# Kernel tuning notes

Measured on AMD Instinct MI355X. Metric: run time of the kernel, lower is better.

The kernel has to match this reference:

```python
import jax, jax.numpy as jnp
import numpy as np

NHEAD = 16


def setup_inputs() -> dict:
    key = jax.random.key(0)
    ks = jax.random.split(key, 6)
    S, B, D = 2048, 2, 1024
    std = float(np.sqrt(6.0 / (D + D)))  # xavier_uniform bound
    inp = {
        "query": jax.random.normal(ks[0], (S, B, D), jnp.float32),
        "key": jax.random.normal(ks[1], (S, B, D), jnp.float32),
        "value": jax.random.normal(ks[2], (S, B, D), jnp.float32),
        "Wq": jax.random.uniform(ks[3], (D, D), jnp.float32, -std, std),
        "bq": jnp.ones((D,), jnp.float32),
        "Wk": jax.random.uniform(ks[4], (D, D), jnp.float32, -std, std),
        "bk": jnp.ones((D,), jnp.float32),
        "Wv": jax.random.uniform(ks[5], (D, D), jnp.float32, -std, std),
        "bv": jnp.ones((D,), jnp.float32),
    }
    return inp


def reference(query, key, value, Wq, bq, Wk, bk, Wv, bv):
    S, B, D = query.shape
    h = NHEAD
    d = D // h
    scale = jnp.asarray(d ** 0.5, query.dtype)
    # projections (nn.Linear: x @ W^T + b)
    q = (query @ Wq.T + bq).reshape(S, B, h, d)
    k = (key @ Wk.T + bk).reshape(S, B, h, d)
    v = (value @ Wv.T + bv).reshape(S, B, h, d)
    # batch_first=False path: scores [b,h,i,j], softmax over j, then AV
    scores = jnp.einsum('ibhd,jbhd->bhij', q, k) / scale
    attn = jax.nn.softmax(scores, axis=-1)
    out = jnp.einsum('bhij,jbhd->ibhd', attn, v).reshape(S, B, D)
    return out
```

## Files before the change

kernel.cpp:

```cpp
#include <hip/hip_runtime.h>
#include <hip/hip_bf16.h>

#define S_LEN 2048
#define BATCH 2
#define DMODEL 1024
#define NHEAD 16
#define HDIM 64
#define MTOT (S_LEN * BATCH)
#define QKV_ELEMS ((size_t)MTOT * DMODEL)
#define XOFF (3 * QKV_ELEMS)
#define WOFF (XOFF + 3 * QKV_ELEMS)
#define WSEG ((size_t)DMODEL * DMODEL)

typedef __bf16 bf16x8 __attribute__((ext_vector_type(8)));
typedef unsigned short u16x8 __attribute__((ext_vector_type(8)));
typedef float f32x4 __attribute__((ext_vector_type(4)));
typedef float f32x16 __attribute__((ext_vector_type(16)));
typedef unsigned int u32x4 __attribute__((ext_vector_type(4)));

__device__ __forceinline__ unsigned short f2bf(float f) {
    unsigned int u = __float_as_uint(f);
    u += 0x7FFFu + ((u >> 16) & 1u);
    return (unsigned short)(u >> 16);
}

__device__ __forceinline__ unsigned int pack2(float lo, float hi) {
    __hip_bfloat162 h = __float22bfloat162_rn(make_float2(lo, hi));
    unsigned int r;
    __builtin_memcpy(&r, &h, 4);
    return r;
}

__device__ __forceinline__ void gload_lds16(const void* g, void* l) {
    __builtin_amdgcn_global_load_lds(
        (const __attribute__((address_space(1))) unsigned int*)g,
        (__attribute__((address_space(3))) unsigned int*)l, 16, 0, 0);
}

__global__ __launch_bounds__(256) void cvt_kernel(
        const float* __restrict__ Xq, const float* __restrict__ Xk,
        const float* __restrict__ Xv, const float* __restrict__ Wq,
        const float* __restrict__ Wk, const float* __restrict__ Wv,
        unsigned short* __restrict__ ws)
{
    const int seg = blockIdx.y;
    const float* src;
    unsigned short* dst;
    int n4;
    if (seg < 3) {
        src = (seg == 0) ? Xq : (seg == 1) ? Xk : Xv;
        dst = ws + XOFF + (size_t)seg * QKV_ELEMS;
        n4  = (int)(QKV_ELEMS / 4);
    } else {
        const int s = seg - 3;
        src = (s == 0) ? Wq : (s == 1) ? Wk : Wv;
        dst = ws + WOFF + (size_t)s * WSEG;
        n4  = (int)(WSEG / 4);
    }
    const int stride = gridDim.x * blockDim.x;
    for (int i = blockIdx.x * blockDim.x + threadIdx.x; i < n4; i += stride) {
        const float4 v = ((const float4*)src)[i];
        uint2 o;
        o.x = pack2(v.x, v.y);
        o.y = pack2(v.z, v.w);
        ((uint2*)dst)[i] = o;
    }
}

#define PBM 128
#define PBN 128
#define PBK 32
#define QSCALE 0.18033688011112042f

__global__ __launch_bounds__(256, 3) void proj_kernel(
        const unsigned short* __restrict__ wsin,
        const float* __restrict__ bq, const float* __restrict__ bk,
        const float* __restrict__ bv, unsigned short* __restrict__ wsout)
{
    const int work = (blockIdx.x & 7) * 96 + (blockIdx.x >> 3);
    const int t    = work >> 8;
    const int rem  = work & 255;
    const int m0   = (rem >> 3) * PBM;
    const int n0   = (rem & 7) * PBN;

    const unsigned short* X = wsin + XOFF + (size_t)t * QKV_ELEMS;
    const unsigned short* W = wsin + WOFF + (size_t)t * WSEG;
    const float* bias = (t == 0) ? bq : (t == 1) ? bk : bv;
    unsigned short* out = wsout + (size_t)t * QKV_ELEMS;
    const float scale = (t == 0) ? QSCALE : 1.0f;

    __shared__ __align__(16) unsigned short Abuf[2][PBM * PBK];
    __shared__ __align__(16) unsigned short Bbuf[2][PBN * PBK];

    const int tid  = threadIdx.x;
    const int wave = tid >> 6;
    const int lane = tid & 63;
    const int lrow = lane & 15;
    const int lg   = lane >> 4;
    const int wr = (wave >> 1) * 64;
    const int wc = (wave & 1) * 64;

    f32x4 acc[4][4];
#pragma unroll
    for (int i = 0; i < 4; ++i)
#pragma unroll
        for (int j = 0; j < 4; ++j)
            acc[i][j] = (f32x4){0.f, 0.f, 0.f, 0.f};

    const int srow_ = tid >> 2;
    const int sc_   = tid & 3;
    const int gsw = (lg ^ (lrow & 3)) * 8;

#pragma unroll
    for (int i0 = 0; i0 < 2; ++i0) {
        const int row = i0 * 64 + srow_;
        const int c   = sc_ ^ (row & 3);
        gload_lds16(X + (size_t)(m0 + row) * DMODEL + c * 8, &Abuf[0][i0 * 2048 + tid * 8]);
        gload_lds16(W + (size_t)(n0 + row) * DMODEL + c * 8, &Bbuf[0][i0 * 2048 + tid * 8]);
    }
    __syncthreads();

    int cur = 0;
    for (int k0 = 0; k0 < DMODEL; k0 += PBK) {
        if (k0 + PBK < DMODEL) {
#pragma unroll
            for (int i0 = 0; i0 < 2; ++i0) {
                const int row = i0 * 64 + srow_;
                const int c   = sc_ ^ (row & 3);
                gload_lds16(X + (size_t)(m0 + row) * DMODEL + k0 + PBK + c * 8,
                            &Abuf[cur ^ 1][i0 * 2048 + tid * 8]);
                gload_lds16(W + (size_t)(n0 + row) * DMODEL + k0 + PBK + c * 8,
                            &Bbuf[cur ^ 1][i0 * 2048 + tid * 8]);
            }
        }

        bf16x8 af[4], bw[4];
#pragma unroll
        for (int i = 0; i < 4; ++i) {
            af[i] = *(const bf16x8*)&Abuf[cur][(wr + i * 16 + lrow) * PBK + gsw];
            bw[i] = *(const bf16x8*)&Bbuf[cur][(wc + i * 16 + lrow) * PBK + gsw];
        }
        __builtin_amdgcn_s_setprio(1);
#pragma unroll
        for (int i = 0; i < 4; ++i)
#pragma unroll
            for (int j = 0; j < 4; ++j)
                acc[i][j] = __builtin_amdgcn_mfma_f32_16x16x32_bf16(af[i], bw[j], acc[i][j], 0, 0, 0);
        __builtin_amdgcn_s_setprio(0);

        __syncthreads();
        cur ^= 1;
    }

#pragma unroll
    for (int j = 0; j < 4; ++j) {
        const int n  = n0 + wc + j * 16 + lrow;
        const float bv_ = bias[n];
        const int h  = n >> 6;
        const int dd = n & 63;
#pragma unroll
        for (int i = 0; i < 4; ++i) {
#pragma unroll
            for (int r = 0; r < 4; ++r) {
                const int m = m0 + wr + i * 16 + lg * 4 + r;
                const int s = m >> 1;
                const int b = m & 1;
                const float v = (acc[i][j][r] + bv_) * scale;
                size_t idx;
                if (t == 2)
                    idx = ((size_t)((b * NHEAD + h) * HDIM + dd)) * S_LEN + s;
                else
                    idx = ((size_t)((b * NHEAD + h) * S_LEN + s)) * HDIM + dd;
                out[idx] = f2bf(v);
            }
        }
    }
}

#define NP 32

__global__ __launch_bounds__(512, 4) void attn_kernel(
        const unsigned short* __restrict__ ws, float* __restrict__ out)
{
    const unsigned short* Qw = ws;
    const unsigned short* Kw = ws + QKV_ELEMS;
    const unsigned short* Vw = ws + 2 * QKV_ELEMS;

    const int bid = blockIdx.x;
    const int idx = bid >> 3;
    const int bh  = (bid & 7) * 4 + (idx >> 4);
    const int q0  = (idx & 15) * 128;

    __shared__ __align__(16) unsigned short SMEM[24576];
    unsigned short* Kb = SMEM;
    unsigned short* Vb = SMEM + 8192;
    unsigned int*   Pb = (unsigned int*)(SMEM + 16384);

    const int tid  = threadIdx.x;
    const int wave = tid >> 6;
    const int lane = tid & 63;
    const int l31  = lane & 31;
    const int half = lane >> 5;
    const int qsub = wave >> 1;
    const int pw   = wave & 1;

    const size_t base = (size_t)bh * S_LEN * HDIM;
    const int qrow = q0 + qsub * 32 + l31;

    bf16x8 qf[4];
#pragma unroll
    for (int c = 0; c < 4; ++c)
        qf[c] = *(const bf16x8*)(Qw + base + (size_t)qrow * HDIM + c * 16 + half * 8);

    bf16x8 ones;
    {
        u16x8 o;
#pragma unroll
        for (int e = 0; e < 8; ++e) o[e] = 0x3F80;
        ones = __builtin_bit_cast(bf16x8, o);
    }

    f32x16 Od0, Od1, Lacc;
#pragma unroll
    for (int i = 0; i < 16; ++i) { Od0[i] = 0.f; Od1[i] = 0.f; Lacc[i] = 0.f; }
    float mrun = -30000.0f;

    unsigned int* PuW = Pb + wave * 512;

    const int stile = tid >> 8;
    const int t256  = tid & 255;
    const int ksrow = t256 >> 3;
    const int ksg   = (t256 & 7) ^ (ksrow & 7);
    const int vrow  = t256 >> 2;
    const int vsg   = (t256 & 3) ^ ((vrow >> 1) & 3);

    int gk[4], gv[2];
#pragma unroll
    for (int c = 0; c < 4; ++c) gk[c] = ((c * 2 + half) ^ (l31 & 7)) * 8;
#pragma unroll
    for (int c = 0; c < 2; ++c) gv[c] = ((c * 2 + half) ^ ((l31 >> 1) & 3)) * 8;

    {
        const int tt = stile;
        gload_lds16(Kw + base + (size_t)(tt * 32 + ksrow) * HDIM + ksg * 8, &Kb[(tt & 3) * 2048 + t256 * 8]);
        gload_lds16(Vw + base + (size_t)vrow * S_LEN + tt * 32 + vsg * 8,   &Vb[(tt & 3) * 2048 + t256 * 8]);
    }
    __syncthreads();

    for (int p = 0; p < NP; ++p) {
        if (p < NP - 1) {
            const int tt = 2 * p + 2 + stile;
            gload_lds16(Kw + base + (size_t)(tt * 32 + ksrow) * HDIM + ksg * 8, &Kb[(tt & 3) * 2048 + t256 * 8]);
            gload_lds16(Vw + base + (size_t)vrow * S_LEN + tt * 32 + vsg * 8,   &Vb[(tt & 3) * 2048 + t256 * 8]);
        }

        const int tm = 2 * p + pw;
        const unsigned short* Klds = &Kb[(tm & 3) * 2048];
        const unsigned short* Vlds = &Vb[(tm & 3) * 2048];

        f32x16 S;
        const float nmrun = -mrun;
#pragma unroll
        for (int i = 0; i < 16; ++i) S[i] = nmrun;
        __builtin_amdgcn_s_setprio(1);
#pragma unroll
        for (int c = 0; c < 4; ++c) {
            const bf16x8 ka = *(const bf16x8*)&Klds[l31 * 64 + gk[c]];
            S = __builtin_amdgcn_mfma_f32_32x32x16_bf16(ka, qf[c], S, 0, 0, 0);
        }
        __builtin_amdgcn_s_setprio(0);

        float m8_[8];
#pragma unroll
        for (int i = 0; i < 8; ++i) m8_[i] = fmaxf(S[i], S[i + 8]);
        const float t0 = fmaxf(fmaxf(m8_[0], m8_[1]), m8_[2]);
        const float t1 = fmaxf(fmaxf(m8_[3], m8_[4]), m8_[5]);
        const float t2 = fmaxf(fmaxf(m8_[6], m8_[7]), t0);
        float mxs = fmaxf(t1, t2);
        mxs = fmaxf(mxs, __shfl_xor(mxs, 32, 64));

        if (!__all(mxs <= 8.0f)) {
            const float d  = fmaxf(mxs, 0.0f);
            const float ex = exp2f(-d);
            mrun += d;
#pragma unroll
            for (int i = 0; i < 16; ++i) S[i] -= d;
            Od0 *= ex;
            Od1 *= ex;
            Lacc[0] *= ex;
        }

#pragma unroll
        for (int i = 0; i < 16; ++i) S[i] = exp2f(S[i]);

#pragma unroll
        for (int u = 0; u < 4; ++u) {
            uint2 two;
            two.x = pack2(S[4 * u],     S[4 * u + 1]);
            two.y = pack2(S[4 * u + 2], S[4 * u + 3]);
            *(uint2*)&PuW[(2 * u + half) * 64 + l31 * 2] = two;
        }
        __asm__ volatile("" ::: "memory");

        __builtin_amdgcn_s_setprio(1);
#pragma unroll
        for (int c = 0; c < 2; ++c) {
            const int row0 = 4 * c + 2 * half;
            const uint2 a = *(const uint2*)&PuW[row0 * 64 + l31 * 2];
            const uint2 b = *(const uint2*)&PuW[(row0 + 1) * 64 + l31 * 2];
            u32x4 pu; pu[0] = a.x; pu[1] = a.y; pu[2] = b.x; pu[3] = b.y;
            const bf16x8 pb = __builtin_bit_cast(bf16x8, pu);
            const bf16x8 va0 = *(const bf16x8*)&Vlds[l31 * 32 + gv[c]];
            const bf16x8 va1 = *(const bf16x8*)&Vlds[(32 + l31) * 32 + gv[c]];
            Od0  = __builtin_amdgcn_mfma_f32_32x32x16_bf16(va0,  pb, Od0,  0, 0, 0);
            Od1  = __builtin_amdgcn_mfma_f32_32x32x16_bf16(va1,  pb, Od1,  0, 0, 0);
            Lacc = __builtin_amdgcn_mfma_f32_32x32x16_bf16(ones, pb, Lacc, 0, 0, 0);
        }
        __builtin_amdgcn_s_setprio(0);

        __syncthreads();
    }

    float* mrg = (float*)SMEM;
    float* reg = mrg + qsub * 2176;
    if (pw) {
        reg[lane]      = mrun;
        reg[64 + lane] = Lacc[0];
#pragma unroll
        for (int i = 0; i < 16; ++i) {
            reg[128 + i * 64 + lane]        = Od0[i];
            reg[128 + (16 + i) * 64 + lane] = Od1[i];
        }
    }
    __syncthreads();
    if (!pw) {
        const float mb = reg[lane];
        const float lb = reg[64 + lane];
        const float ms = fmaxf(mrun, mb);
        const float sa = exp2f(mrun - ms);
        const float sb = exp2f(mb - ms);
        const float linv = 1.0f / (Lacc[0] * sa + lb * sb);

        const int bb = bh >> 4;
        const int hh = bh & 15;
        float* op = out + (size_t)qrow * (BATCH * DMODEL) + bb * DMODEL + hh * HDIM;
#pragma unroll
        for (int gg = 0; gg < 4; ++gg) {
            const int d0 = gg * 8 + half * 4;
            float4 v0, v1;
            v0.x = (Od0[gg * 4 + 0] * sa + reg[128 + (gg * 4 + 0) * 64 + lane] * sb) * linv;
            v0.y = (Od0[gg * 4 + 1] * sa + reg[128 + (gg * 4 + 1) * 64 + lane] * sb) * linv;
            v0.z = (Od0[gg * 4 + 2] * sa + reg[128 + (gg * 4 + 2) * 64 + lane] * sb) * linv;
            v0.w = (Od0[gg * 4 + 3] * sa + reg[128 + (gg * 4 + 3) * 64 + lane] * sb) * linv;
            v1.x = (Od1[gg * 4 + 0] * sa + reg[128 + (16 + gg * 4 + 0) * 64 + lane] * sb) * linv;
            v1.y = (Od1[gg * 4 + 1] * sa + reg[128 + (16 + gg * 4 + 1) * 64 + lane] * sb) * linv;
            v1.z = (Od1[gg * 4 + 2] * sa + reg[128 + (16 + gg * 4 + 2) * 64 + lane] * sb) * linv;
            v1.w = (Od1[gg * 4 + 3] * sa + reg[128 + (16 + gg * 4 + 3) * 64 + lane] * sb) * linv;
            *(float4*)(op + d0)      = v0;
            *(float4*)(op + 32 + d0) = v1;
        }
    }
}

extern "C" void kernel_launch(void* const* d_in, const int* in_sizes, int n_in,
                              void* d_out, int out_size, void* d_ws, size_t ws_size,
                              hipStream_t stream) {
    const float* q  = (const float*)d_in[0];
    const float* k  = (const float*)d_in[1];
    const float* v  = (const float*)d_in[2];
    const float* Wq = (const float*)d_in[3];
    const float* bq = (const float*)d_in[4];
    const float* Wk = (const float*)d_in[5];
    const float* bk = (const float*)d_in[6];
    const float* Wv = (const float*)d_in[7];
    const float* bv = (const float*)d_in[8];
    unsigned short* ws = (unsigned short*)d_ws;
    float* out = (float*)d_out;

    cvt_kernel<<<dim3(1024, 6), dim3(256), 0, stream>>>(q, k, v, Wq, Wk, Wv, ws);
    proj_kernel<<<dim3(768), dim3(256), 0, stream>>>(ws, bq, bk, bv, ws);
    attn_kernel<<<dim3(512), dim3(512), 0, stream>>>(ws, out);
}
```

Measured before the change: 131.5 us.

## Deepen K/V LDS prefetch to triple buffering with partial vmcnt waits

Grows the K/V shared-memory ring from four to six tile slots so loads run two iterations ahead instead of one. Each loop end now waits only for the older pair of global-to-LDS loads (vmcnt(2)) before the barrier, replacing a full __syncthreads drain, so memory latency can hide behind more compute. The cost is more LDS per block (64 KB vs 48 KB), which may lower occupancy, plus modular slot indexing.

```diff
diff --git a/kernel.cpp b/kernel.cpp
--- a/kernel.cpp
+++ b/kernel.cpp
@@ -191,10 +191,10 @@
     const int bh  = (bid & 7) * 4 + (idx >> 4);
     const int q0  = (idx & 15) * 128;
 
-    __shared__ __align__(16) unsigned short SMEM[24576];
+    __shared__ __align__(16) unsigned short SMEM[32768];
     unsigned short* Kb = SMEM;
-    unsigned short* Vb = SMEM + 8192;
-    unsigned int*   Pb = (unsigned int*)(SMEM + 16384);
+    unsigned short* Vb = SMEM + 12288;
+    unsigned int*   Pb = (unsigned int*)(SMEM + 24576);
 
     const int tid  = threadIdx.x;
     const int wave = tid >> 6;
@@ -241,22 +241,29 @@
     for (int c = 0; c < 2; ++c) gv[c] = ((c * 2 + half) ^ ((l31 >> 1) & 3)) * 8;
 
     {
-        const int tt = stile;
-        gload_lds16(Kw + base + (size_t)(tt * 32 + ksrow) * HDIM + ksg * 8, &Kb[(tt & 3) * 2048 + t256 * 8]);
-        gload_lds16(Vw + base + (size_t)vrow * S_LEN + tt * 32 + vsg * 8,   &Vb[(tt & 3) * 2048 + t256 * 8]);
-    }
-    __syncthreads();
-
+        const int tt0 = stile;
+        gload_lds16(Kw + base + (size_t)(tt0 * 32 + ksrow) * HDIM + ksg * 8, &Kb[tt0 * 2048 + t256 * 8]);
+        gload_lds16(Vw + base + (size_t)vrow * S_LEN + tt0 * 32 + vsg * 8,   &Vb[tt0 * 2048 + t256 * 8]);
+        const int tt1 = stile + 2;
+        gload_lds16(Kw + base + (size_t)(tt1 * 32 + ksrow) * HDIM + ksg * 8, &Kb[tt1 * 2048 + t256 * 8]);
+        gload_lds16(Vw + base + (size_t)vrow * S_LEN + tt1 * 32 + vsg * 8,   &Vb[tt1 * 2048 + t256 * 8]);
+    }
+    asm volatile("s_waitcnt vmcnt(2)" ::: "memory");
+    __builtin_amdgcn_s_barrier();
+
+    int c3 = 0;
     for (int p = 0; p < NP; ++p) {
-        if (p < NP - 1) {
-            const int tt = 2 * p + 2 + stile;
-            gload_lds16(Kw + base + (size_t)(tt * 32 + ksrow) * HDIM + ksg * 8, &Kb[(tt & 3) * 2048 + t256 * 8]);
-            gload_lds16(Vw + base + (size_t)vrow * S_LEN + tt * 32 + vsg * 8,   &Vb[(tt & 3) * 2048 + t256 * 8]);
-        }
-
-        const int tm = 2 * p + pw;
-        const unsigned short* Klds = &Kb[(tm & 3) * 2048];
-        const unsigned short* Vlds = &Vb[(tm & 3) * 2048];
+        if (p < NP - 2) {
+            const int tt = 2 * p + 4 + stile;
+            int slot = 2 * c3 + 4 + stile;
+            if (slot >= 6) slot -= 6;
+            gload_lds16(Kw + base + (size_t)(tt * 32 + ksrow) * HDIM + ksg * 8, &Kb[slot * 2048 + t256 * 8]);
+            gload_lds16(Vw + base + (size_t)vrow * S_LEN + tt * 32 + vsg * 8,   &Vb[slot * 2048 + t256 * 8]);
+        }
+
+        const int rslot = 2 * c3 + pw;
+        const unsigned short* Klds = &Kb[rslot * 2048];
+        const unsigned short* Vlds = &Vb[rslot * 2048];
 
         f32x16 S;
         const float nmrun = -mrun;
@@ -318,7 +325,11 @@
         }
         __builtin_amdgcn_s_setprio(0);
 
-        __syncthreads();
+        if (p < NP - 2) asm volatile("s_waitcnt vmcnt(2)" ::: "memory");
+        else            asm volatile("s_waitcnt vmcnt(0)" ::: "memory");
+        __builtin_amdgcn_s_barrier();
+
+        c3 = (c3 == 2) ? 0 : c3 + 1;
     }
 
     float* mrg = (float*)SMEM;
```

After: 134.0 us. About the same (+1.9%).
